# Kernel tuning notes

Measured on AMD Instinct MI355X. Metric: run time of the kernel, lower is better.

Reference implementation:

```python
import jax, jax.numpy as jnp
import numpy as np

DIM = 384
HEADS = 8


def setup_inputs() -> dict:
    key = jax.random.key(0)
    ks = jax.random.split(key, 6)
    B, H, W = 8, 64, 64
    N, C = H * W, DIM
    s = 0.02  # init scale for weights
    return {
        "x": jax.random.normal(ks[0], (B, N, C), jnp.float32),
        # depthwise conv: OIHW with feature_group_count=C -> [C,1,3,3]
        "w_sr": jax.random.normal(ks[1], (C, 1, 3, 3), jnp.float32) * s,
        "b_sr": jax.random.normal(ks[2], (C,), jnp.float32) * s,
        "ln_g": jnp.ones((C,), jnp.float32),
        "ln_b": jnp.zeros((C,), jnp.float32),
        # linears stored [in, out] (torch stores [out,in]; random so equivalent)
        "w_qkv": jax.random.normal(ks[3], (C, 3 * C), jnp.float32) * s,
        "w_proj": jax.random.normal(ks[4], (C, C), jnp.float32) * s,
        "b_proj": jax.random.normal(ks[5], (C,), jnp.float32) * s,
        "H": 64,
        "W": 64,
    }


def reference(x, w_sr, b_sr, ln_g, ln_b, w_qkv, w_proj, b_proj, H, W):
    B, N, C = x.shape
    h = HEADS
    d = C // h
    shortcut = x

    # --- depthwise conv branch: sr(x) -> LN -> GELU -> residual add ---
    x_img = x.transpose(0, 2, 1).reshape(B, C, H, W)
    x_sr = jax.lax.conv_general_dilated(
        x_img, w_sr, window_strides=(1, 1), padding="SAME",
        dimension_numbers=("NCHW", "OIHW", "NCHW"), feature_group_count=C,
    ) + b_sr[None, :, None, None]
    x_sr = x_sr.reshape(B, C, N).transpose(0, 2, 1)  # [B, N, C]
    mu = x_sr.mean(-1, keepdims=True)
    var = x_sr.var(-1, keepdims=True)
    xn = (x_sr - mu) * jax.lax.rsqrt(var + 1e-5) * ln_g + ln_b
    x = x + jax.nn.gelu(xn, approximate=False)  # torch GELU is erf-based

    # --- linear attention ---
    qkv = (x @ w_qkv).reshape(B, N, 3, h, d)
    q = qkv[:, :, 0].transpose(0, 2, 1, 3)  # [B, h, N, d]
    k = qkv[:, :, 1].transpose(0, 2, 1, 3)
    v = qkv[:, :, 2].transpose(0, 2, 1, 3)
    q = jax.nn.softmax(q, axis=-2)  # softmax over sequence dim N
    k = jax.nn.softmax(k, axis=-1)  # softmax over head_dim
    ctx = jnp.einsum("bhnd,bhne->bhde", k, v)          # [B, h, d, d]
    attn = jnp.einsum("bhnd,bhde->bhne", q, ctx)       # [B, h, N, d]
    attn = attn.transpose(0, 2, 1, 3).reshape(B, N, C)

    out = attn @ w_proj + b_proj
    return out + shortcut
```

## Files before the change

### kernel.cpp

```cpp
#include <hip/hip_runtime.h>

typedef unsigned short u16;
typedef u16   u16x4  __attribute__((ext_vector_type(4)));
typedef u16   u16x8  __attribute__((ext_vector_type(8)));
typedef short short8 __attribute__((ext_vector_type(8)));
typedef float floatx4 __attribute__((ext_vector_type(4)));
typedef float f4     __attribute__((ext_vector_type(4)));

typedef const __attribute__((address_space(1))) unsigned gu32;
typedef __attribute__((address_space(3))) unsigned lu32;

#define BB 8
#define NN 4096
#define CC 384

__device__ __forceinline__ u16 f2bf(float f){
  unsigned u = __float_as_uint(f);
  u += 0x7FFFu + ((u >> 16) & 1u);
  return (u16)(u >> 16);
}

__global__ __launch_bounds__(384) void k_pre(
    const float* __restrict__ x, const float* __restrict__ w_sr, const float* __restrict__ b_sr,
    const float* __restrict__ ln_g, const float* __restrict__ ln_b,
    const float* __restrict__ wqkv, u16* __restrict__ xa16, u16* __restrict__ WT,
    float* __restrict__ Z)
{
  const int blk = blockIdx.x;

  if (blk >= 4204) {
    int off = (blk - 4204) * 1536 + ((int)threadIdx.x << 2);
    const f4 zz = {0.f, 0.f, 0.f, 0.f};
    *(f4*)(Z + off) = zz;
    return;
  }

  if (blk >= 4096) {
    const int pb = blk - 4096;
    const int cg = pb % 18, kg = pb / 18;
    const int c0 = cg << 6, k0 = kg << 6;
    const int tid = threadIdx.x;
    __shared__ u16 t[64][72];
    if (tid < 256) {
#pragma unroll
      for (int i = 0; i < 4; i++) {
        int idx = tid + (i << 8);
        int r = idx >> 4, c4 = (idx & 15) << 2;
        f4 v = *(const f4*)(wqkv + (size_t)(k0 + r) * 1152 + c0 + c4);
#pragma unroll
        for (int j = 0; j < 4; j++) t[c4 + j][r] = f2bf(v[j]);
      }
    }
    __syncthreads();
    if (tid < 256) {
#pragma unroll
      for (int i = 0; i < 2; i++) {
        int idx = tid + (i << 8);
        int c = idx >> 3, j = (idx & 7) << 3;
        *(u16x8*)(WT + (size_t)(c0 + c) * 384 + k0 + j) = *(const u16x8*)&t[c][j];
      }
    }
    return;
  }

  const int b = blk >> 9;
  const int hh = (blk >> 3) & 63;
  const int ww0 = (blk & 7) << 3;
  const int c = threadIdx.x;

  float wgt[9];
#pragma unroll
  for (int i = 0; i < 9; i++) wgt[i] = w_sr[c * 9 + i];
  const float lg = ln_g[c], lb = ln_b[c];
  const float bias = b_sr[c];

  float rowv[3][10];
#pragma unroll
  for (int r = 0; r < 3; r++) {
    int y = hh + r - 1;
    bool yok = (unsigned)y < 64u;
#pragma unroll
    for (int j = 0; j < 10; j++) {
      int xx = ww0 + j - 1;
      bool ok = yok && ((unsigned)xx < 64u);
      rowv[r][j] = ok ? x[((size_t)((b << 12) + (y << 6) + xx)) * CC + c] : 0.f;
    }
  }

  float acc[8];
#pragma unroll
  for (int p = 0; p < 8; p++) {
    float a = bias;
#pragma unroll
    for (int r = 0; r < 3; r++)
#pragma unroll
      for (int j = 0; j < 3; j++)
        a += rowv[r][p + j] * wgt[r * 3 + j];
    acc[p] = a;
  }

  __shared__ float ls1[6][8], ls2[6][8], mb[2][8];
  const int wid = threadIdx.x >> 6, lane = threadIdx.x & 63;
#pragma unroll
  for (int p = 0; p < 8; p++) {
    float s1 = acc[p], s2 = acc[p] * acc[p];
#pragma unroll
    for (int o = 32; o > 0; o >>= 1) { s1 += __shfl_down(s1, o); s2 += __shfl_down(s2, o); }
    if (lane == 0) { ls1[wid][p] = s1; ls2[wid][p] = s2; }
  }
  __syncthreads();
  if (threadIdx.x < 8) {
    int p = threadIdx.x;
    float a = 0.f, q = 0.f;
#pragma unroll
    for (int i = 0; i < 6; i++) { a += ls1[i][p]; q += ls2[i][p]; }
    float mean = a * (1.0f / CC);
    float var  = q * (1.0f / CC) - mean * mean;
    mb[0][p] = mean; mb[1][p] = rsqrtf(var + 1e-5f);
  }
  __syncthreads();
#pragma unroll
  for (int p = 0; p < 8; p++) {
    float xn = (acc[p] - mb[0][p]) * mb[1][p] * lg + lb;
    float g  = 0.5f * xn * (1.0f + erff(xn * 0.70710678118654752f));
    size_t pix = (size_t)(b << 12) + (hh << 6) + ww0 + p;
    xa16[pix * CC + c] = f2bf(rowv[1][p + 1] + g);
  }
}

__global__ __launch_bounds__(512) void k_qkv(
    const u16* __restrict__ xa16, const u16* __restrict__ WT, float* __restrict__ S,
    u16* __restrict__ K16T, u16* __restrict__ V16T, u16* __restrict__ P16)
{
  const int rt = blockIdx.x;
  const int g  = blockIdx.y;
  const int b  = rt >> 6;
  const int n0 = rt << 6;
  const int tid = threadIdx.x;
  const int wv = tid >> 6, lane = tid & 63, l15 = lane & 15, quad = lane >> 4;
  const int wc = wv;

  __shared__ __attribute__((aligned(16))) u16 lA[2][64][32];
  __shared__ __attribute__((aligned(16))) u16 lB[2][384][32];

  const u16* Bbase = WT + (size_t)((g == 2) ? 0 : (384 + g * 384)) * 384;
  const int sw8 = (quad ^ ((l15 >> 1) & 3)) << 3;

  floatx4 acc[12];
  const floatx4 z = {0.f, 0.f, 0.f, 0.f};
#pragma unroll
  for (int i = 0; i < 12; i++) acc[i] = z;

  auto stage = [&](int bi, int k0) {
    if (wv < 4) {
      int cl = (wv << 4) + (lane >> 2);
      int sc = ((lane & 3) ^ ((cl >> 1) & 3)) << 3;
      __builtin_amdgcn_global_load_lds((gu32*)(xa16 + (size_t)(n0 + cl) * 384 + k0 + sc),
                                       (lu32*)&lA[bi][wv << 4][0], 16, 0, 0);
    }
#pragma unroll
    for (int i = 0; i < 3; i++) {
      int j = wv * 3 + i;
      int cl = (j << 4) + (lane >> 2);
      int sc = ((lane & 3) ^ ((cl >> 1) & 3)) << 3;
      __builtin_amdgcn_global_load_lds((gu32*)(Bbase + (size_t)cl * 384 + k0 + sc),
                                       (lu32*)&lB[bi][j << 4][0], 16, 0, 0);
    }
  };

  stage(0, 0);
  __syncthreads();

  for (int t = 0; t < 12; t++) {
    const int cur = t & 1;
    if (t < 11) stage(cur ^ 1, (t + 1) << 5);
    short8 af[4], bf[3];
#pragma unroll
    for (int mi = 0; mi < 4; mi++) af[mi] = *(const short8*)&lA[cur][(mi << 4) + l15][sw8];
#pragma unroll
    for (int ni = 0; ni < 3; ni++) bf[ni] = *(const short8*)&lB[cur][wc * 48 + (ni << 4) + l15][sw8];
#pragma unroll
    for (int mi = 0; mi < 4; mi++)
#pragma unroll
      for (int ni = 0; ni < 3; ni++)
        acc[mi * 3 + ni] = __builtin_amdgcn_mfma_f32_16x16x32_bf16(af[mi], bf[ni], acc[mi * 3 + ni], 0, 0, 0);
    __syncthreads();
  }

  if (g == 0) {
#pragma unroll
    for (int mi = 0; mi < 4; mi++)
#pragma unroll
      for (int rr = 0; rr < 4; rr++) {
        float x0 = acc[mi * 3 + 0][rr], x1 = acc[mi * 3 + 1][rr], x2 = acc[mi * 3 + 2][rr];
        float m = fmaxf(fmaxf(x0, x1), x2);
#pragma unroll
        for (int o = 8; o >= 1; o >>= 1) m = fmaxf(m, __shfl_xor(m, o));
        float e0 = expf(x0 - m), e1 = expf(x1 - m), e2 = expf(x2 - m);
        float s = e0 + e1 + e2;
#pragma unroll
        for (int o = 8; o >= 1; o >>= 1) s += __shfl_xor(s, o);
        float inv = 1.0f / s;
        acc[mi * 3 + 0][rr] = e0 * inv; acc[mi * 3 + 1][rr] = e1 * inv; acc[mi * 3 + 2][rr] = e2 * inv;
      }
  }

  if (g == 2) {
#pragma unroll
    for (int ni = 0; ni < 3; ni++) {
      int col = wc * 48 + (ni << 4) + l15;
      float s = 0.f;
#pragma unroll
      for (int mi = 0; mi < 4; mi++) {
        int rowb = n0 + (mi << 4) + (quad << 2);
        float e0 = expf(acc[mi * 3 + ni][0]), e1 = expf(acc[mi * 3 + ni][1]);
        float e2 = expf(acc[mi * 3 + ni][2]), e3 = expf(acc[mi * 3 + ni][3]);
        P16[(size_t)(rowb + 0) * 384 + col] = f2bf(e0);
        P16[(size_t)(rowb + 1) * 384 + col] = f2bf(e1);
        P16[(size_t)(rowb + 2) * 384 + col] = f2bf(e2);
        P16[(size_t)(rowb + 3) * 384 + col] = f2bf(e3);
        s += e0 + e1 + e2 + e3;
      }
      s += __shfl_down(s, 32);
      s += __shfl_down(s, 16);
      if (lane < 16) atomicAdd(&S[b * 384 + wc * 48 + (ni << 4) + lane], s);
    }
  } else {
    u16* dst = g ? V16T : K16T;
    const int nl = ((rt & 63) << 6) + (quad << 2);
#pragma unroll
    for (int mi = 0; mi < 4; mi++)
#pragma unroll
      for (int ni = 0; ni < 3; ni++) {
        int hd = wc * 48 + (ni << 4) + l15;
        u16x4 v4 = { f2bf(acc[mi * 3 + ni][0]), f2bf(acc[mi * 3 + ni][1]),
                     f2bf(acc[mi * 3 + ni][2]), f2bf(acc[mi * 3 + ni][3]) };
        *(u16x4*)(dst + ((size_t)b * 384 + hd) * 4096 + nl + (mi << 4)) = v4;
      }
  }
}

__global__ __launch_bounds__(256) void k_ctx(
    const u16* __restrict__ K16T, const u16* __restrict__ V16T, float* __restrict__ ctx)
{
  const int bh = blockIdx.x;
  const int b = bh >> 3, h = bh & 7;
  const int n0 = blockIdx.y << 8;
  const int tid = threadIdx.x;
  const int wv = tid >> 6, lane = tid & 63, l15 = lane & 15, quad = lane >> 4;

  __shared__ __attribute__((aligned(16))) char smem[50688];
  u16 (*lkT)[264] = (u16(*)[264])smem;
  u16 (*lvT)[264] = (u16(*)[264])(smem + 25344);
  float (*pctx)[2304] = (float(*)[2304])smem;

#pragma unroll
  for (int i = 0; i < 6; i++) {
    int idx = tid + (i << 8);
    int d = idx >> 5, c8 = (idx & 31) << 3;
    *(u16x8*)&lkT[d][c8] = *(const u16x8*)(K16T + ((size_t)b * 384 + h * 48 + d) * 4096 + n0 + c8);
    *(u16x8*)&lvT[d][c8] = *(const u16x8*)(V16T + ((size_t)b * 384 + h * 48 + d) * 4096 + n0 + c8);
  }
  __syncthreads();

  floatx4 c2[9];
  const floatx4 z = {0.f, 0.f, 0.f, 0.f};
#pragma unroll
  for (int i = 0; i < 9; i++) c2[i] = z;
#pragma unroll
  for (int kk2 = 0; kk2 < 2; kk2++) {
    int rb = (wv << 6) + (kk2 << 5) + (quad << 3);
    short8 ak[3], av[3];
#pragma unroll
    for (int t = 0; t < 3; t++) {
      ak[t] = *(const short8*)&lkT[(t << 4) + l15][rb];
      av[t] = *(const short8*)&lvT[(t << 4) + l15][rb];
    }
#pragma unroll
    for (int dt = 0; dt < 3; dt++)
#pragma unroll
      for (int et = 0; et < 3; et++)
        c2[dt * 3 + et] = __builtin_amdgcn_mfma_f32_16x16x32_bf16(ak[dt], av[et], c2[dt * 3 + et], 0, 0, 0);
  }
  __syncthreads();

#pragma unroll
  for (int dt = 0; dt < 3; dt++)
#pragma unroll
    for (int et = 0; et < 3; et++)
#pragma unroll
      for (int rr = 0; rr < 4; rr++) {
        int d = (dt << 4) + (quad << 2) + rr;
        int e = (et << 4) + l15;
        pctx[wv][d * 48 + e] = c2[dt * 3 + et][rr];
      }
  __syncthreads();
#pragma unroll
  for (int i = 0; i < 9; i++) {
    int cell = tid + (i << 8);
    float s = pctx[0][cell] + pctx[1][cell] + pctx[2][cell] + pctx[3][cell];
    atomicAdd(&ctx[(size_t)bh * 2304 + cell], s);
  }
}

__global__ __launch_bounds__(256) void k_w2(
    const float* __restrict__ ctx, const float* __restrict__ S,
    const float* __restrict__ wp, u16* __restrict__ W2T)
{
  const int bh = blockIdx.x;
  const int b = bh >> 3, h = bh & 7;
  const int c0 = blockIdx.y << 7;
  const int tid = threadIdx.x;
  __shared__ float rs[48];
  __shared__ float c2[48][48];
  __shared__ float lwp[48][128];
  __shared__ u16 tr[128][48];
  if (tid < 48) rs[tid] = 1.0f / S[b * 384 + h * 48 + tid];
  __syncthreads();
#pragma unroll
  for (int i = 0; i < 9; i++) {
    int cell = tid + (i << 8);
    int d = cell / 48, e = cell - d * 48;
    c2[d][e] = ctx[(size_t)bh * 2304 + cell] * rs[d];
  }
#pragma unroll
  for (int i = 0; i < 24; i++) {
    int idx = tid + (i << 8);
    int e = idx >> 7, c = idx & 127;
    lwp[e][c] = wp[(size_t)(h * 48 + e) * 384 + c0 + c];
  }
  __syncthreads();
  const int c = tid & 127;
  const int dbase = tid >> 7;
#pragma unroll
  for (int it = 0; it < 24; it++) {
    int d = (it << 1) + dbase;
    float s = 0.f;
#pragma unroll
    for (int e = 0; e < 48; e++) s += c2[d][e] * lwp[e][c];
    tr[c][d] = f2bf(s);
  }
  __syncthreads();
  const int cc = tid >> 1, half = tid & 1;
#pragma unroll
  for (int i = 0; i < 3; i++) {
    u16x8 v = *(const u16x8*)&tr[cc][half * 24 + (i << 3)];
    *(u16x8*)(W2T + ((size_t)b * 384 + c0 + cc) * 384 + h * 48 + half * 24 + (i << 3)) = v;
  }
}

__global__ __launch_bounds__(512) void k_qproj(
    const u16* __restrict__ P16, const u16* __restrict__ W2T,
    const float* __restrict__ bias, const float* __restrict__ x, float* __restrict__ out)
{
  const int bm = blockIdx.x;
  const int b = bm >> 6;
  const int n0 = bm << 6;
  const int tid = threadIdx.x;
  const int wv = tid >> 6, lane = tid & 63, l15 = lane & 15, quad = lane >> 4;
  const int wc = wv;

  __shared__ __attribute__((aligned(16))) u16 lA[2][64][32];
  __shared__ __attribute__((aligned(16))) u16 lB[2][384][32];

  const u16* Bbase = W2T + (size_t)b * 384 * 384;
  const int sw8 = (quad ^ ((l15 >> 1) & 3)) << 3;

  floatx4 acc[12];
  const floatx4 z = {0.f, 0.f, 0.f, 0.f};
#pragma unroll
  for (int i = 0; i < 12; i++) acc[i] = z;

  auto stage = [&](int bi, int k0) {
    if (wv < 4) {
      int cl = (wv << 4) + (lane >> 2);
      int sc = ((lane & 3) ^ ((cl >> 1) & 3)) << 3;
      __builtin_amdgcn_global_load_lds((gu32*)(P16 + (size_t)(n0 + cl) * 384 + k0 + sc),
                                       (lu32*)&lA[bi][wv << 4][0], 16, 0, 0);
    }
#pragma unroll
    for (int i = 0; i < 3; i++) {
      int j = wv * 3 + i;
      int cl = (j << 4) + (lane >> 2);
      int sc = ((lane & 3) ^ ((cl >> 1) & 3)) << 3;
      __builtin_amdgcn_global_load_lds((gu32*)(Bbase + (size_t)cl * 384 + k0 + sc),
                                       (lu32*)&lB[bi][j << 4][0], 16, 0, 0);
    }
  };

  stage(0, 0);
  __syncthreads();

  for (int t = 0; t < 12; t++) {
    const int cur = t & 1;
    if (t < 11) stage(cur ^ 1, (t + 1) << 5);
    short8 af[4], bf[3];
#pragma unroll
    for (int mi = 0; mi < 4; mi++) af[mi] = *(const short8*)&lA[cur][(mi << 4) + l15][sw8];
#pragma unroll
    for (int ni = 0; ni < 3; ni++) bf[ni] = *(const short8*)&lB[cur][wc * 48 + (ni << 4) + l15][sw8];
#pragma unroll
    for (int mi = 0; mi < 4; mi++)
#pragma unroll
      for (int ni = 0; ni < 3; ni++)
        acc[mi * 3 + ni] = __builtin_amdgcn_mfma_f32_16x16x32_bf16(af[mi], bf[ni], acc[mi * 3 + ni], 0, 0, 0);
    __syncthreads();
  }

#pragma unroll
  for (int ni = 0; ni < 3; ni++) {
    int col = wc * 48 + (ni << 4) + l15;
    float bc = bias[col];
#pragma unroll
    for (int mi = 0; mi < 4; mi++) {
#pragma unroll
      for (int rr = 0; rr < 4; rr++) {
        int row = n0 + (mi << 4) + (quad << 2) + rr;
        out[(size_t)row * 384 + col] = acc[mi * 3 + ni][rr] + bc + x[(size_t)row * 384 + col];
      }
    }
  }
}

extern "C" void kernel_launch(void* const* d_in, const int* in_sizes, int n_in,
                              void* d_out, int out_size, void* d_ws, size_t ws_size,
                              hipStream_t stream)
{
  const float* x      = (const float*)d_in[0];
  const float* w_sr   = (const float*)d_in[1];
  const float* b_sr   = (const float*)d_in[2];
  const float* ln_g   = (const float*)d_in[3];
  const float* ln_b   = (const float*)d_in[4];
  const float* w_qkv  = (const float*)d_in[5];
  const float* w_proj = (const float*)d_in[6];
  const float* b_proj = (const float*)d_in[7];
  float* out = (float*)d_out;

  float* S   = (float*)d_ws;
  float* ctx = (float*)((char*)d_ws + 12288);
  u16*   WT  = (u16*)((char*)d_ws + 602112);
  u16*   W2T = (u16*)((char*)d_ws + 1486848);
  u16*   xa16= (u16*)((char*)d_ws + 3846144);
  u16*   P16 = (u16*)((char*)d_ws + 29011968);
  u16*   K16T= (u16*)d_out;
  u16*   V16T= (u16*)d_out + (size_t)8 * 384 * 4096;

  k_pre<<<4302, 384, 0, stream>>>(x, w_sr, b_sr, ln_g, ln_b, w_qkv, xa16, WT, (float*)d_ws);
  k_qkv<<<dim3(512, 3), 512, 0, stream>>>(xa16, WT, S, K16T, V16T, P16);
  k_ctx<<<dim3(64, 16), 256, 0, stream>>>(K16T, V16T, ctx);
  k_w2<<<dim3(64, 3), 256, 0, stream>>>(ctx, S, w_proj, W2T);
  k_qproj<<<512, 512, 0, stream>>>(P16, W2T, b_proj, x, out);
}
```

Measured before the change: 256.2 us.

## Fuse K·V context computation into QKV GEMM kernel, drop K/V round trip

The ctx kernel is removed: blocks with gy==0 now compute the K GEMM (with its head-dim softmax) and then the V GEMM, stage both as bf16 tiles in swizzled shared memory, and accumulate the per-head K^T V product directly into ctx with atomics. This avoids writing K and V transposed to global memory and reading them back. The GEMM staging also changes from async global-to-LDS double buffering to register prefetch with a single buffer. The trade-offs are many more fine-grained atomics on ctx (one per element per block, with no in-block reduction), a larger LDS footprint, and serialised GEMMs within a block.

```diff
diff --git a/kernel.cpp b/kernel.cpp
--- a/kernel.cpp
+++ b/kernel.cpp
@@ -130,64 +130,83 @@
 
 __global__ __launch_bounds__(512) void k_qkv(
     const u16* __restrict__ xa16, const u16* __restrict__ WT, float* __restrict__ S,
-    u16* __restrict__ K16T, u16* __restrict__ V16T, u16* __restrict__ P16)
+    float* __restrict__ ctx, u16* __restrict__ P16)
 {
-  const int rt = blockIdx.x;
-  const int g  = blockIdx.y;
-  const int b  = rt >> 6;
-  const int n0 = rt << 6;
+  const int rt = blockIdx.x, gy = blockIdx.y;
+  const int b = rt >> 6, n0 = rt << 6;
   const int tid = threadIdx.x;
   const int wv = tid >> 6, lane = tid & 63, l15 = lane & 15, quad = lane >> 4;
   const int wc = wv;
 
-  __shared__ __attribute__((aligned(16))) u16 lA[2][64][32];
-  __shared__ __attribute__((aligned(16))) u16 lB[2][384][32];
-
-  const u16* Bbase = WT + (size_t)((g == 2) ? 0 : (384 + g * 384)) * 384;
+  __shared__ __attribute__((aligned(16))) char smem[77824];
+  u16 (*lA)[32] = (u16(*)[32])smem;
+  u16 (*lB)[32] = (u16(*)[32])(smem + 4096);
+  u16* vTw = (u16*)smem + wv * 1536;
+  u16* kTw = (u16*)(smem + 28672) + wv * 3072;
+
   const int sw8 = (quad ^ ((l15 >> 1) & 3)) << 3;
+  const int clA = tid >> 2, cA_ = tid & 3;
+  const int swA = (cA_ ^ ((clA >> 1) & 3)) << 3;
 
   floatx4 acc[12];
   const floatx4 z = {0.f, 0.f, 0.f, 0.f};
-#pragma unroll
-  for (int i = 0; i < 12; i++) acc[i] = z;
-
-  auto stage = [&](int bi, int k0) {
-    if (wv < 4) {
-      int cl = (wv << 4) + (lane >> 2);
-      int sc = ((lane & 3) ^ ((cl >> 1) & 3)) << 3;
-      __builtin_amdgcn_global_load_lds((gu32*)(xa16 + (size_t)(n0 + cl) * 384 + k0 + sc),
-                                       (lu32*)&lA[bi][wv << 4][0], 16, 0, 0);
-    }
+
+  auto run_gemm = [&](const u16* Bb) {
+#pragma unroll
+    for (int i = 0; i < 12; i++) acc[i] = z;
+    u16x8 ra, rb[3];
+    if (tid < 256) ra = *(const u16x8*)(xa16 + (size_t)(n0 + clA) * 384 + (cA_ << 3));
 #pragma unroll
     for (int i = 0; i < 3; i++) {
-      int j = wv * 3 + i;
-      int cl = (j << 4) + (lane >> 2);
-      int sc = ((lane & 3) ^ ((cl >> 1) & 3)) << 3;
-      __builtin_amdgcn_global_load_lds((gu32*)(Bbase + (size_t)cl * 384 + k0 + sc),
-                                       (lu32*)&lB[bi][j << 4][0], 16, 0, 0);
+      int idx = tid + (i << 9);
+      rb[i] = *(const u16x8*)(Bb + (size_t)(idx >> 2) * 384 + ((idx & 3) << 3));
+    }
+    if (tid < 256) *(u16x8*)&lA[clA][swA] = ra;
+#pragma unroll
+    for (int i = 0; i < 3; i++) {
+      int idx = tid + (i << 9);
+      int cl = idx >> 2;
+      *(u16x8*)&lB[cl][((idx & 3) ^ ((cl >> 1) & 3)) << 3] = rb[i];
+    }
+    __syncthreads();
+
+    for (int t = 0; t < 12; t++) {
+      const bool pf = (t < 11);
+      const int kn = (t + 1) << 5;
+      if (pf) {
+        if (tid < 256) ra = *(const u16x8*)(xa16 + (size_t)(n0 + clA) * 384 + kn + (cA_ << 3));
+#pragma unroll
+        for (int i = 0; i < 3; i++) {
+          int idx = tid + (i << 9);
+          rb[i] = *(const u16x8*)(Bb + (size_t)(idx >> 2) * 384 + kn + ((idx & 3) << 3));
+        }
+      }
+      short8 af[4], bf[3];
+#pragma unroll
+      for (int mi = 0; mi < 4; mi++) af[mi] = *(const short8*)&lA[(mi << 4) + l15][sw8];
+#pragma unroll
+      for (int ni = 0; ni < 3; ni++) bf[ni] = *(const short8*)&lB[wc * 48 + (ni << 4) + l15][sw8];
+#pragma unroll
+      for (int mi = 0; mi < 4; mi++)
+#pragma unroll
+        for (int ni = 0; ni < 3; ni++)
+          acc[mi * 3 + ni] = __builtin_amdgcn_mfma_f32_16x16x32_bf16(af[mi], bf[ni], acc[mi * 3 + ni], 0, 0, 0);
+      __syncthreads();
+      if (pf) {
+        if (tid < 256) *(u16x8*)&lA[clA][swA] = ra;
+#pragma unroll
+        for (int i = 0; i < 3; i++) {
+          int idx = tid + (i << 9);
+          int cl = idx >> 2;
+          *(u16x8*)&lB[cl][((idx & 3) ^ ((cl >> 1) & 3)) << 3] = rb[i];
+        }
+        __syncthreads();
+      }
     }
   };
 
-  stage(0, 0);
-  __syncthreads();
-
-  for (int t = 0; t < 12; t++) {
-    const int cur = t & 1;
-    if (t < 11) stage(cur ^ 1, (t + 1) << 5);
-    short8 af[4], bf[3];
-#pragma unroll
-    for (int mi = 0; mi < 4; mi++) af[mi] = *(const short8*)&lA[cur][(mi << 4) + l15][sw8];
-#pragma unroll
-    for (int ni = 0; ni < 3; ni++) bf[ni] = *(const short8*)&lB[cur][wc * 48 + (ni << 4) + l15][sw8];
-#pragma unroll
-    for (int mi = 0; mi < 4; mi++)
-#pragma unroll
-      for (int ni = 0; ni < 3; ni++)
-        acc[mi * 3 + ni] = __builtin_amdgcn_mfma_f32_16x16x32_bf16(af[mi], bf[ni], acc[mi * 3 + ni], 0, 0, 0);
-    __syncthreads();
-  }
-
-  if (g == 0) {
+  if (gy == 0) {
+    run_gemm(WT + (size_t)384 * 384);
 #pragma unroll
     for (int mi = 0; mi < 4; mi++)
 #pragma unroll
@@ -203,9 +222,61 @@
         float inv = 1.0f / s;
         acc[mi * 3 + 0][rr] = e0 * inv; acc[mi * 3 + 1][rr] = e1 * inv; acc[mi * 3 + 2][rr] = e2 * inv;
       }
-  }
-
-  if (g == 2) {
+#pragma unroll
+    for (int mi = 0; mi < 4; mi++)
+#pragma unroll
+      for (int ni = 0; ni < 3; ni++) {
+        int d = (ni << 4) + l15;
+        int idx = (((d << 6) + (mi << 4) + (quad << 2)) ^ ((d & 7) << 3));
+        u16x4 v4 = { f2bf(acc[mi * 3 + ni][0]), f2bf(acc[mi * 3 + ni][1]),
+                     f2bf(acc[mi * 3 + ni][2]), f2bf(acc[mi * 3 + ni][3]) };
+        *(u16x4*)&kTw[idx] = v4;
+      }
+    run_gemm(WT + (size_t)768 * 384);
+
+    floatx4 c2[9];
+#pragma unroll
+    for (int i = 0; i < 9; i++) c2[i] = z;
+#pragma unroll
+    for (int c = 0; c < 2; c++) {
+#pragma unroll
+      for (int m2 = 0; m2 < 2; m2++) {
+        int mi = (c << 1) + m2;
+#pragma unroll
+        for (int ni = 0; ni < 3; ni++) {
+          int e = (ni << 4) + l15;
+          int idx = (((e << 5) + (m2 << 4) + (quad << 2)) ^ ((e & 3) << 3));
+          u16x4 v4 = { f2bf(acc[mi * 3 + ni][0]), f2bf(acc[mi * 3 + ni][1]),
+                       f2bf(acc[mi * 3 + ni][2]), f2bf(acc[mi * 3 + ni][3]) };
+          *(u16x4*)&vTw[idx] = v4;
+        }
+      }
+      short8 ak[3], av[3];
+#pragma unroll
+      for (int t3 = 0; t3 < 3; t3++) {
+        int d = (t3 << 4) + l15;
+        ak[t3] = *(const short8*)&kTw[(((d << 6) + (c << 5) + (quad << 3)) ^ ((d & 7) << 3))];
+        av[t3] = *(const short8*)&vTw[(((d << 5) + (quad << 3)) ^ ((d & 3) << 3))];
+      }
+#pragma unroll
+      for (int dt = 0; dt < 3; dt++)
+#pragma unroll
+        for (int et = 0; et < 3; et++)
+          c2[dt * 3 + et] = __builtin_amdgcn_mfma_f32_16x16x32_bf16(ak[dt], av[et], c2[dt * 3 + et], 0, 0, 0);
+    }
+    const int bh = (b << 3) + wv;
+#pragma unroll
+    for (int dt = 0; dt < 3; dt++)
+#pragma unroll
+      for (int et = 0; et < 3; et++)
+#pragma unroll
+        for (int rr = 0; rr < 4; rr++) {
+          int d = (dt << 4) + (quad << 2) + rr;
+          int e = (et << 4) + l15;
+          atomicAdd(&ctx[(size_t)bh * 2304 + d * 48 + e], c2[dt * 3 + et][rr]);
+        }
+  } else {
+    run_gemm(WT);
 #pragma unroll
     for (int ni = 0; ni < 3; ni++) {
       int col = wc * 48 + (ni << 4) + l15;
@@ -225,81 +296,6 @@
       s += __shfl_down(s, 16);
       if (lane < 16) atomicAdd(&S[b * 384 + wc * 48 + (ni << 4) + lane], s);
     }
-  } else {
-    u16* dst = g ? V16T : K16T;
-    const int nl = ((rt & 63) << 6) + (quad << 2);
-#pragma unroll
-    for (int mi = 0; mi < 4; mi++)
-#pragma unroll
-      for (int ni = 0; ni < 3; ni++) {
-        int hd = wc * 48 + (ni << 4) + l15;
-        u16x4 v4 = { f2bf(acc[mi * 3 + ni][0]), f2bf(acc[mi * 3 + ni][1]),
-                     f2bf(acc[mi * 3 + ni][2]), f2bf(acc[mi * 3 + ni][3]) };
-        *(u16x4*)(dst + ((size_t)b * 384 + hd) * 4096 + nl + (mi << 4)) = v4;
-      }
-  }
-}
-
-__global__ __launch_bounds__(256) void k_ctx(
-    const u16* __restrict__ K16T, const u16* __restrict__ V16T, float* __restrict__ ctx)
-{
-  const int bh = blockIdx.x;
-  const int b = bh >> 3, h = bh & 7;
-  const int n0 = blockIdx.y << 8;
-  const int tid = threadIdx.x;
-  const int wv = tid >> 6, lane = tid & 63, l15 = lane & 15, quad = lane >> 4;
-
-  __shared__ __attribute__((aligned(16))) char smem[50688];
-  u16 (*lkT)[264] = (u16(*)[264])smem;
-  u16 (*lvT)[264] = (u16(*)[264])(smem + 25344);
-  float (*pctx)[2304] = (float(*)[2304])smem;
-
-#pragma unroll
-  for (int i = 0; i < 6; i++) {
-    int idx = tid + (i << 8);
-    int d = idx >> 5, c8 = (idx & 31) << 3;
-    *(u16x8*)&lkT[d][c8] = *(const u16x8*)(K16T + ((size_t)b * 384 + h * 48 + d) * 4096 + n0 + c8);
-    *(u16x8*)&lvT[d][c8] = *(const u16x8*)(V16T + ((size_t)b * 384 + h * 48 + d) * 4096 + n0 + c8);
-  }
-  __syncthreads();
-
-  floatx4 c2[9];
-  const floatx4 z = {0.f, 0.f, 0.f, 0.f};
-#pragma unroll
-  for (int i = 0; i < 9; i++) c2[i] = z;
-#pragma unroll
-  for (int kk2 = 0; kk2 < 2; kk2++) {
-    int rb = (wv << 6) + (kk2 << 5) + (quad << 3);
-    short8 ak[3], av[3];
-#pragma unroll
-    for (int t = 0; t < 3; t++) {
-      ak[t] = *(const short8*)&lkT[(t << 4) + l15][rb];
-      av[t] = *(const short8*)&lvT[(t << 4) + l15][rb];
-    }
-#pragma unroll
-    for (int dt = 0; dt < 3; dt++)
-#pragma unroll
-      for (int et = 0; et < 3; et++)
-        c2[dt * 3 + et] = __builtin_amdgcn_mfma_f32_16x16x32_bf16(ak[dt], av[et], c2[dt * 3 + et], 0, 0, 0);
-  }
-  __syncthreads();
-
-#pragma unroll
-  for (int dt = 0; dt < 3; dt++)
-#pragma unroll
-    for (int et = 0; et < 3; et++)
-#pragma unroll
-      for (int rr = 0; rr < 4; rr++) {
-        int d = (dt << 4) + (quad << 2) + rr;
-        int e = (et << 4) + l15;
-        pctx[wv][d * 48 + e] = c2[dt * 3 + et][rr];
-      }
-  __syncthreads();
-#pragma unroll
-  for (int i = 0; i < 9; i++) {
-    int cell = tid + (i << 8);
-    float s = pctx[0][cell] + pctx[1][cell] + pctx[2][cell] + pctx[3][cell];
-    atomicAdd(&ctx[(size_t)bh * 2304 + cell], s);
   }
 }
 
@@ -442,12 +438,9 @@
   u16*   W2T = (u16*)((char*)d_ws + 1486848);
   u16*   xa16= (u16*)((char*)d_ws + 3846144);
   u16*   P16 = (u16*)((char*)d_ws + 29011968);
-  u16*   K16T= (u16*)d_out;
-  u16*   V16T= (u16*)d_out + (size_t)8 * 384 * 4096;
 
   k_pre<<<4302, 384, 0, stream>>>(x, w_sr, b_sr, ln_g, ln_b, w_qkv, xa16, WT, (float*)d_ws);
-  k_qkv<<<dim3(512, 3), 512, 0, stream>>>(xa16, WT, S, K16T, V16T, P16);
-  k_ctx<<<dim3(64, 16), 256, 0, stream>>>(K16T, V16T, ctx);
+  k_qkv<<<dim3(512, 2), 512, 0, stream>>>(xa16, WT, S, ctx, P16);
   k_w2<<<dim3(64, 3), 256, 0, stream>>>(ctx, S, w_proj, W2T);
   k_qproj<<<512, 512, 0, stream>>>(P16, W2T, b_proj, x, out);
 }
```

Result: no change. 260.0 us (+1.5%).
